# Kernel optimization log

Measured on AMD Instinct MI355X. Metric: run time of the kernel, lower is better.

The kernel has to match this reference:

```python
import jax, jax.numpy as jnp
import numpy as np
import math

SLIDING_WINDOW = 1024  # matches init kwarg

def setup_inputs() -> dict:
    key = jax.random.key(0)
    ks = jax.random.split(key, 6)
    B, S, Hq, Hkv, D = 1, 2048, 32, 8, 128
    NUM_PAGES, STRIDE = 300, 16
    q = jax.random.normal(ks[0], (B, S, Hq, D), dtype=jnp.float32)
    k = jax.random.normal(ks[1], (B, S, Hkv, D), dtype=jnp.float32)
    v = jax.random.normal(ks[2], (B, S, Hkv, D), dtype=jnp.float32)
    sink = jax.random.normal(ks[3], (Hq,), dtype=jnp.float32)
    cache_state = jnp.zeros((NUM_PAGES, STRIDE, 2, Hkv, D), dtype=jnp.float32)
    seq_block_ids = jax.random.randint(ks[4], (B, S // STRIDE), 0, NUM_PAGES, dtype=jnp.int64)
    return {"q": q, "k": k, "v": v, "sink": sink,
            "cache_state": cache_state, "seq_block_ids": seq_block_ids}


def reference(q, k, v, sink, cache_state, seq_block_ids):
    B, S, Hq, D = q.shape
    Hkv = k.shape[2]
    stride = cache_state.shape[1]

    # --- paged cache write (prefill side effect) ---
    kv = jnp.stack([k, v], axis=2)                       # [B,S,2,Hkv,D]
    pages = kv.reshape(B * (S // stride), stride, 2, Hkv, D)
    _ = cache_state.at[seq_block_ids.reshape(-1)].set(pages)

    # --- decomposed attention: matmul + mask + softmax(+sink) + matmul ---
    rep = Hq // Hkv
    ke = jnp.repeat(k, rep, axis=2)                      # [B,S,Hq,D] (GQA expand)
    ve = jnp.repeat(v, rep, axis=2)
    scale = 1.0 / math.sqrt(D)
    scores = jnp.einsum('bihd,bjhd->bhij', q, ke) * scale  # [B,Hq,S,S]

    i = jnp.arange(S)[:, None]
    j = jnp.arange(S)[None, :]
    allowed = (j <= i) & (i - j < SLIDING_WINDOW)        # causal + sliding window
    neg = jnp.finfo(scores.dtype).min
    logits = jnp.where(allowed, scores, neg)

    # attention sink: extra per-head logit appended; contributes to denominator only
    sink_l = jnp.broadcast_to(sink[None, :, None, None], (B, Hq, S, 1))
    probs = jax.nn.softmax(jnp.concatenate([logits, sink_l], axis=-1), axis=-1)[..., :S]

    out = jnp.einsum('bhij,bjhd->bihd', probs, ve)       # [B,S,Hq,D]
    return out
```

## Files before the change

kernel.cpp:

```cpp
#include <hip/hip_runtime.h>
#include <hip/hip_bf16.h>


#define S_LEN 2048
#define DH    128
#define HQ    32
#define HKV   8
#define WIN   1024
#define BR    64
#define BC    32
#define NT    (S_LEN / BC)
#define FM    16.0f
#define TILE_CH 512

typedef unsigned short u16;
typedef __attribute__((ext_vector_type(8))) short  short8;
typedef __attribute__((ext_vector_type(4))) float  floatx4;
typedef __attribute__((ext_vector_type(4))) unsigned int uintx4;

__device__ __forceinline__ unsigned rne1(float a) {
    unsigned u = __float_as_uint(a);
    return (u + 0x7FFFu + ((u >> 16) & 1u)) >> 16;
}
__device__ __forceinline__ unsigned rne_pk(float a, float b) {
    return rne1(a) | (rne1(b) << 16);
}
__device__ __forceinline__ unsigned cvt_pk(float a, float b) {
    unsigned r;
    asm("v_cvt_pk_bf16_f32 %0, %1, %2" : "=v"(r) : "v"(a), "v"(b));
    return r;
}

__global__ __launch_bounds__(256) void pack_kv(const float* __restrict__ kg,
                                               const float* __restrict__ vg,
                                               u16* __restrict__ kp,
                                               u16* __restrict__ vtp)
{
    __shared__ float Vs[BC][DH + 1];
    const int b   = blockIdx.x;
    const int hk  = b >> 6;
    const int jt  = b & 63;
    const int tid = threadIdx.x;
    const int j0  = jt * BC;

    #pragma unroll
    for (int t = 0; t < 4; t++) {
        int idx = tid + t * 256;
        int j   = idx >> 5;
        int dc  = idx & 31;
        floatx4 f = *(const floatx4*)(vg + ((size_t)(j0 + j) * HKV + hk) * DH + dc * 4);
        Vs[j][dc * 4 + 0] = f[0]; Vs[j][dc * 4 + 1] = f[1];
        Vs[j][dc * 4 + 2] = f[2]; Vs[j][dc * 4 + 3] = f[3];
    }

    u16* kpt = kp + (size_t)b * TILE_CH * 8;
    #pragma unroll
    for (int t = 0; t < 2; t++) {
        int c = tid + t * 256;
        int row = c >> 4, cc = c & 15;
        const float* p = kg + ((size_t)(j0 + row) * HKV + hk) * DH + cc * 8;
        floatx4 f0 = *(const floatx4*)p;
        floatx4 f1 = *(const floatx4*)(p + 4);
        int pc = (((row >> 4) * 4 + (cc >> 2)) << 6) | ((cc & 3) << 4) | (row & 15);
        *(uintx4*)(kpt + pc * 8) =
            (uintx4){rne_pk(f0[0], f0[1]), rne_pk(f0[2], f0[3]),
                     rne_pk(f1[0], f1[1]), rne_pk(f1[2], f1[3])};
    }
    __syncthreads();

    u16* vpt = vtp + (size_t)b * TILE_CH * 8;
    #pragma unroll
    for (int t = 0; t < 2; t++) {
        int q  = tid + t * 256;
        int dd = q >> 2, c = q & 3;
        unsigned w0 = rne_pk(Vs[c * 4 + 0][dd], Vs[c * 4 + 16][dd]);
        unsigned w1 = rne_pk(Vs[c * 4 + 1][dd], Vs[c * 4 + 17][dd]);
        unsigned w2 = rne_pk(Vs[c * 4 + 2][dd], Vs[c * 4 + 18][dd]);
        unsigned w3 = rne_pk(Vs[c * 4 + 3][dd], Vs[c * 4 + 19][dd]);
        int qp = ((dd >> 4) << 6) | (c << 4) | (dd & 15);
        *(uintx4*)(vpt + qp * 8) = (uintx4){w0, w1, w2, w3};
    }
}

__launch_bounds__(256, 5)
__global__ void fa_kernel(const float* __restrict__ qg,
                          const u16* __restrict__ kp,
                          const u16* __restrict__ vtp,
                          const float* __restrict__ sg,
                          float* __restrict__ outg)
{
    __shared__ __align__(16) u16 Kt[2][TILE_CH * 8];
    __shared__ __align__(16) u16 Vt[2][TILE_CH * 8];

    const int tid  = threadIdx.x;
    const int w    = tid >> 6;
    const int lane = tid & 63;
    const int quad = lane >> 4;
    const int l16  = lane & 15;

    const int bid  = blockIdx.x;
    const int hk   = bid & 7;
    const int idx  = bid >> 3;
    const int hrem = idx & 3;
    const int u5   = (idx >> 2) & 7;
    const int t4   = idx >> 5;
    const int qbt[4] = {u5, 15 - u5, 16 + u5, 31 - u5};
    const int qb   = qbt[t4];
    const int h    = hk * 4 + hrem;

    const int i0 = qb * BR;
    const int m0 = i0 + w * 16;

    short8 qf[4];
    {
        const float* qrow = qg + ((size_t)(m0 + l16) * HQ + h) * DH;
        #pragma unroll
        for (int kk = 0; kk < 4; kk++) {
            const float* p = qrow + kk * 32 + quad * 8;
            floatx4 f0 = *(const floatx4*)p;
            floatx4 f1 = *(const floatx4*)(p + 4);
            uintx4 uq = (uintx4){cvt_pk(f0[0], f0[1]), cvt_pk(f0[2], f0[3]),
                                 cvt_pk(f1[0], f1[1]), cvt_pk(f1[2], f1[3])};
            qf[kk] = *(short8*)&uq;
        }
    }

    const int lane8 = lane * 8;

    floatx4 acc[8];
    #pragma unroll
    for (int i = 0; i < 8; i++) acc[i] = (floatx4){0.f, 0.f, 0.f, 0.f};
    float l_sum = 0.f;

    const int ci  = m0 + l16;
    const int qb4 = quad * 4;

    int jlo = i0 - (WIN - 1); if (jlo < 0) jlo = 0;
    const int jt_lo = jlo >> 5;
    const int jt_hi = (i0 + BR - 1) >> 5;

    const float SC2 = 0.08838834764831845f * 1.4426950408889634f;

    const int ch0 = w * 64 + lane;
    auto stage = [&](int bb, int jt) {
        const u16* kpt = kp  + ((size_t)(hk * NT + jt)) * TILE_CH * 8;
        const u16* vpt = vtp + ((size_t)(hk * NT + jt)) * TILE_CH * 8;
        #pragma unroll
        for (int it = 0; it < 2; it++) {
            int ch = ch0 + it * 256;
            __builtin_amdgcn_global_load_lds(
                (const __attribute__((address_space(1))) unsigned*)(kpt + ch * 8),
                (__attribute__((address_space(3))) unsigned*)(&Kt[bb][ch * 8]), 16, 0, 0);
            __builtin_amdgcn_global_load_lds(
                (const __attribute__((address_space(1))) unsigned*)(vpt + ch * 8),
                (__attribute__((address_space(3))) unsigned*)(&Vt[bb][ch * 8]), 16, 0, 0);
        }
    };

    stage(0, jt_lo);
    int bb = 0;

    for (int jt = jt_lo; jt <= jt_hi; jt++) {
        const int j0 = jt << 5;

        __syncthreads();

        if (jt < jt_hi) stage(bb ^ 1, jt + 1);

        floatx4 ss[2];
        ss[0] = (floatx4){0.f, 0.f, 0.f, 0.f};
        ss[1] = (floatx4){0.f, 0.f, 0.f, 0.f};
        #pragma unroll
        for (int kk = 0; kk < 4; kk++) {
            short8 kf0 = *(const short8*)(&Kt[bb][(kk << 9) + lane8]);
            short8 kf1 = *(const short8*)(&Kt[bb][((4 + kk) << 9) + lane8]);
            ss[0] = __builtin_amdgcn_mfma_f32_16x16x32_bf16(kf0, qf[kk], ss[0], 0, 0, 0);
            ss[1] = __builtin_amdgcn_mfma_f32_16x16x32_bf16(kf1, qf[kk], ss[1], 0, 0, 0);
        }

        float p[2][4];
        const bool interior = (j0 + (BC - 1) <= i0) && (j0 >= i0 + BR - WIN);
        if (interior) {
            #pragma unroll
            for (int n = 0; n < 2; n++)
                #pragma unroll
                for (int r = 0; r < 4; r++)
                    p[n][r] = exp2f(fmaf(ss[n][r], SC2, -FM));
        } else {
            const int dj = ci - j0;
            #pragma unroll
            for (int n = 0; n < 2; n++)
                #pragma unroll
                for (int r = 0; r < 4; r++) {
                    int t = n * 16 + qb4 + r;
                    bool a = (t <= dj) && (t > dj - WIN);
                    p[n][r] = a ? exp2f(fmaf(ss[n][r], SC2, -FM)) : 0.f;
                }
        }
        l_sum += ((p[0][0] + p[0][1]) + (p[0][2] + p[0][3]))
               + ((p[1][0] + p[1][1]) + (p[1][2] + p[1][3]));

        uintx4 upf = (uintx4){cvt_pk(p[0][0], p[1][0]), cvt_pk(p[0][1], p[1][1]),
                              cvt_pk(p[0][2], p[1][2]), cvt_pk(p[0][3], p[1][3])};
        short8 pf = *(short8*)&upf;

        #pragma unroll
        for (int nf = 0; nf < 8; nf++) {
            short8 vf = *(const short8*)(&Vt[bb][(nf << 9) + lane8]);
            acc[nf] = __builtin_amdgcn_mfma_f32_16x16x32_bf16(pf, vf, acc[nf], 0, 0, 0);
        }
        bb ^= 1;
    }

    l_sum += __shfl_xor(l_sum, 16);
    l_sum += __shfl_xor(l_sum, 32);
    const float sk2 = exp2f(fmaf(sg[h], 1.4426950408889634f, -FM));
    float inv_r[4];
    #pragma unroll
    for (int r = 0; r < 4; r++) {
        float Lr = __shfl(l_sum, qb4 + r);
        inv_r[r] = 1.f / (Lr + sk2);
    }
    #pragma unroll
    for (int nf = 0; nf < 8; nf++) {
        int d = nf * 16 + l16;
        #pragma unroll
        for (int r = 0; r < 4; r++) {
            int ig = m0 + qb4 + r;
            outg[((size_t)ig * HQ + h) * DH + d] = acc[nf][r] * inv_r[r];
        }
    }
}

__launch_bounds__(256, 4)
__global__ void fa_fallback(const float* __restrict__ qg,
                            const float* __restrict__ kg,
                            const float* __restrict__ vg,
                            const float* __restrict__ sg,
                            float* __restrict__ outg)
{
    __shared__ __align__(16) u16 Kt[BC * DH];
    __shared__ __align__(16) u16 Vt[DH * BC];
    __shared__ __align__(16) u16 Pb[BR * 40];

    const int tid  = threadIdx.x;
    const int w    = tid >> 6;
    const int lane = tid & 63;
    const int quad = lane >> 4;
    const int l16  = lane & 15;

    const int qb = blockIdx.x / HQ;
    const int h  = blockIdx.x % HQ;
    const int hk = h >> 2;
    const int i0 = qb * BR;
    const int m0 = i0 + w * 16;

    short8 qf[4];
    {
        const float* qrow = qg + ((size_t)(m0 + l16) * HQ + h) * DH;
        #pragma unroll
        for (int kk = 0; kk < 4; kk++) {
            const float* p = qrow + kk * 32 + quad * 8;
            floatx4 f0 = *(const floatx4*)p;
            floatx4 f1 = *(const floatx4*)(p + 4);
            uintx4 u = (uintx4){rne_pk(f0[0], f0[1]), rne_pk(f0[2], f0[3]),
                                rne_pk(f1[0], f1[1]), rne_pk(f1[2], f1[3])};
            qf[kk] = *(short8*)&u;
        }
    }

    floatx4 acc[8];
    #pragma unroll
    for (int i = 0; i < 8; i++) acc[i] = (floatx4){0.f, 0.f, 0.f, 0.f};
    float l_part[4] = {0.f, 0.f, 0.f, 0.f};

    int jlo = i0 - (WIN - 1); if (jlo < 0) jlo = 0;
    const int jt_lo = jlo >> 5;
    const int jt_hi = (i0 + BR - 1) >> 5;
    const float SC2 = 0.08838834764831845f * 1.4426950408889634f;

    for (int jt = jt_lo; jt <= jt_hi; jt++) {
        const int j0 = jt << 5;
        __syncthreads();
        #pragma unroll
        for (int it = 0; it < 2; it++) {
            int g   = tid + 256 * it;
            int row = g >> 4, cc = g & 15;
            int pc  = (row << 4) | (cc ^ (row & 7));
            const float* kpp = kg + ((size_t)(j0 + row) * HKV + hk) * DH + cc * 8;
            floatx4 f0 = *(const floatx4*)kpp;
            floatx4 f1 = *(const floatx4*)(kpp + 4);
            *(uintx4*)(&Kt[pc * 8]) =
                (uintx4){rne_pk(f0[0], f0[1]), rne_pk(f0[2], f0[3]),
                         rne_pk(f1[0], f1[1]), rne_pk(f1[2], f1[3])};
        }
        #pragma unroll
        for (int it = 0; it < 2; it++) {
            int g  = tid + 256 * it;
            int d  = g & 127, jc = g >> 7;
            const float* vp = vg + ((size_t)(j0 + jc * 8) * HKV + hk) * DH + d;
            float e0 = vp[0 * HKV * DH], e1 = vp[1 * HKV * DH];
            float e2 = vp[2 * HKV * DH], e3 = vp[3 * HKV * DH];
            float e4 = vp[4 * HKV * DH], e5 = vp[5 * HKV * DH];
            float e6 = vp[6 * HKV * DH], e7 = vp[7 * HKV * DH];
            int pc = (d << 2) | (jc ^ ((d >> 2) & 3));
            *(uintx4*)(&Vt[pc * 8]) =
                (uintx4){rne_pk(e0, e1), rne_pk(e2, e3), rne_pk(e4, e5), rne_pk(e6, e7)};
        }
        __syncthreads();

        floatx4 sc[2];
        sc[0] = (floatx4){0.f, 0.f, 0.f, 0.f};
        sc[1] = (floatx4){0.f, 0.f, 0.f, 0.f};
        #pragma unroll
        for (int kk = 0; kk < 4; kk++) {
            #pragma unroll
            for (int n = 0; n < 2; n++) {
                int row = n * 16 + l16;
                int cc  = kk * 4 + quad;
                int pc  = (row << 4) | (cc ^ (row & 7));
                short8 kf = *(const short8*)(&Kt[pc * 8]);
                sc[n] = __builtin_amdgcn_mfma_f32_16x16x32_bf16(qf[kk], kf, sc[n], 0, 0, 0);
            }
        }
        #pragma unroll
        for (int r = 0; r < 4; r++) {
            int   i_g = m0 + quad * 4 + r;
            int   jg0 = j0 + l16, jg1 = j0 + 16 + l16;
            bool  a0  = (jg0 <= i_g) && (i_g - jg0 < WIN);
            bool  a1  = (jg1 <= i_g) && (i_g - jg1 < WIN);
            float p0  = a0 ? exp2f(fmaf(sc[0][r], SC2, -FM)) : 0.f;
            float p1  = a1 ? exp2f(fmaf(sc[1][r], SC2, -FM)) : 0.f;
            l_part[r] += p0 + p1;
            int prow = w * 16 + quad * 4 + r;
            *(unsigned*)(&Pb[prow * 40 + 2 * l16]) = rne_pk(p0, p1);
        }
        {
            short8 pf = *(const short8*)(&Pb[(w * 16 + l16) * 40 + quad * 8]);
            #pragma unroll
            for (int nf = 0; nf < 8; nf++) {
                int dd = nf * 16 + l16;
                int qp = (dd << 2) | (quad ^ ((dd >> 2) & 3));
                short8 vf = *(const short8*)(&Vt[qp * 8]);
                acc[nf] = __builtin_amdgcn_mfma_f32_16x16x32_bf16(pf, vf, acc[nf], 0, 0, 0);
            }
        }
    }

    const float sk2 = exp2f(fmaf(sg[h], 1.4426950408889634f, -FM));
    float inv[4];
    #pragma unroll
    for (int r = 0; r < 4; r++) {
        float l = l_part[r];
        #pragma unroll
        for (int off = 1; off < 16; off <<= 1)
            l += __shfl_xor(l, off);
        inv[r] = 1.f / (l + sk2);
    }
    #pragma unroll
    for (int nf = 0; nf < 8; nf++) {
        int d = nf * 16 + l16;
        #pragma unroll
        for (int r = 0; r < 4; r++) {
            int ig = m0 + quad * 4 + r;
            outg[((size_t)ig * HQ + h) * DH + d] = acc[nf][r] * inv[r];
        }
    }
}

extern "C" void kernel_launch(void* const* d_in, const int* in_sizes, int n_in,
                              void* d_out, int out_size, void* d_ws, size_t ws_size,
                              hipStream_t stream) {
    const float* q  = (const float*)d_in[0];
    const float* k  = (const float*)d_in[1];
    const float* v  = (const float*)d_in[2];
    const float* sk = (const float*)d_in[3];
    float* out = (float*)d_out;

    const size_t tile_elems = (size_t)HKV * NT * TILE_CH * 8;
    const size_t need = 2 * tile_elems * sizeof(u16);

    if (ws_size >= need) {
        u16* kp  = (u16*)d_ws;
        u16* vtp = kp + tile_elems;
        pack_kv<<<dim3(HKV * NT), 256, 0, stream>>>(k, v, kp, vtp);
        fa_kernel<<<dim3((S_LEN / BR) * HQ), 256, 0, stream>>>(q, kp, vtp, sk, out);
    } else {
        fa_fallback<<<dim3((S_LEN / BR) * HQ), 256, 0, stream>>>(q, k, v, sk, out);
    }
}
```

Before: 155.8 us.

## Halve warps per block, give each warp two 16-row query tiles

The attention block now runs 2 warps of 64 lanes instead of 4, and each warp handles 32 query rows as two 16-row MFMA tiles. Each K and V fragment read from LDS is reused across both query tiles, which halves LDS reads per unit of MFMA work. In exchange, per-thread register use roughly doubles for accumulators and Q fragments, and each block has fewer waves to hide latency; launch bounds change to (128, 2). Staging now issues four global-to-LDS loads per thread instead of two.

```diff
diff --git a/kernel.cpp b/kernel.cpp
--- a/kernel.cpp
+++ b/kernel.cpp
@@ -82,7 +82,7 @@
     }
 }
 
-__launch_bounds__(256, 5)
+__launch_bounds__(128, 2)
 __global__ void fa_kernel(const float* __restrict__ qg,
                           const u16* __restrict__ kp,
                           const u16* __restrict__ vtp,
@@ -109,11 +109,12 @@
     const int h    = hk * 4 + hrem;
 
     const int i0 = qb * BR;
-    const int m0 = i0 + w * 16;
-
-    short8 qf[4];
-    {
-        const float* qrow = qg + ((size_t)(m0 + l16) * HQ + h) * DH;
+    const int m0 = i0 + w * 32;
+
+    short8 qf[2][4];
+    #pragma unroll
+    for (int m = 0; m < 2; m++) {
+        const float* qrow = qg + ((size_t)(m0 + m * 16 + l16) * HQ + h) * DH;
         #pragma unroll
         for (int kk = 0; kk < 4; kk++) {
             const float* p = qrow + kk * 32 + quad * 8;
@@ -121,18 +122,19 @@
             floatx4 f1 = *(const floatx4*)(p + 4);
             uintx4 uq = (uintx4){cvt_pk(f0[0], f0[1]), cvt_pk(f0[2], f0[3]),
                                  cvt_pk(f1[0], f1[1]), cvt_pk(f1[2], f1[3])};
-            qf[kk] = *(short8*)&uq;
+            qf[m][kk] = *(short8*)&uq;
         }
     }
 
     const int lane8 = lane * 8;
 
-    floatx4 acc[8];
-    #pragma unroll
-    for (int i = 0; i < 8; i++) acc[i] = (floatx4){0.f, 0.f, 0.f, 0.f};
-    float l_sum = 0.f;
-
-    const int ci  = m0 + l16;
+    floatx4 acc[2][8];
+    #pragma unroll
+    for (int m = 0; m < 2; m++)
+        #pragma unroll
+        for (int i = 0; i < 8; i++) acc[m][i] = (floatx4){0.f, 0.f, 0.f, 0.f};
+    float l_sum[2] = {0.f, 0.f};
+
     const int qb4 = quad * 4;
 
     int jlo = i0 - (WIN - 1); if (jlo < 0) jlo = 0;
@@ -141,13 +143,12 @@
 
     const float SC2 = 0.08838834764831845f * 1.4426950408889634f;
 
-    const int ch0 = w * 64 + lane;
     auto stage = [&](int bb, int jt) {
         const u16* kpt = kp  + ((size_t)(hk * NT + jt)) * TILE_CH * 8;
         const u16* vpt = vtp + ((size_t)(hk * NT + jt)) * TILE_CH * 8;
         #pragma unroll
-        for (int it = 0; it < 2; it++) {
-            int ch = ch0 + it * 256;
+        for (int it = 0; it < 4; it++) {
+            int ch = tid + it * 128;
             __builtin_amdgcn_global_load_lds(
                 (const __attribute__((address_space(1))) unsigned*)(kpt + ch * 8),
                 (__attribute__((address_space(3))) unsigned*)(&Kt[bb][ch * 8]), 16, 0, 0);
@@ -167,67 +168,80 @@
 
         if (jt < jt_hi) stage(bb ^ 1, jt + 1);
 
-        floatx4 ss[2];
-        ss[0] = (floatx4){0.f, 0.f, 0.f, 0.f};
-        ss[1] = (floatx4){0.f, 0.f, 0.f, 0.f};
+        floatx4 ss[2][2];
+        #pragma unroll
+        for (int n = 0; n < 2; n++) {
+            ss[n][0] = (floatx4){0.f, 0.f, 0.f, 0.f};
+            ss[n][1] = (floatx4){0.f, 0.f, 0.f, 0.f};
+        }
         #pragma unroll
         for (int kk = 0; kk < 4; kk++) {
             short8 kf0 = *(const short8*)(&Kt[bb][(kk << 9) + lane8]);
             short8 kf1 = *(const short8*)(&Kt[bb][((4 + kk) << 9) + lane8]);
-            ss[0] = __builtin_amdgcn_mfma_f32_16x16x32_bf16(kf0, qf[kk], ss[0], 0, 0, 0);
-            ss[1] = __builtin_amdgcn_mfma_f32_16x16x32_bf16(kf1, qf[kk], ss[1], 0, 0, 0);
-        }
-
-        float p[2][4];
+            ss[0][0] = __builtin_amdgcn_mfma_f32_16x16x32_bf16(kf0, qf[0][kk], ss[0][0], 0, 0, 0);
+            ss[0][1] = __builtin_amdgcn_mfma_f32_16x16x32_bf16(kf0, qf[1][kk], ss[0][1], 0, 0, 0);
+            ss[1][0] = __builtin_amdgcn_mfma_f32_16x16x32_bf16(kf1, qf[0][kk], ss[1][0], 0, 0, 0);
+            ss[1][1] = __builtin_amdgcn_mfma_f32_16x16x32_bf16(kf1, qf[1][kk], ss[1][1], 0, 0, 0);
+        }
+
+        short8 pf[2];
         const bool interior = (j0 + (BC - 1) <= i0) && (j0 >= i0 + BR - WIN);
-        if (interior) {
-            #pragma unroll
-            for (int n = 0; n < 2; n++)
+        #pragma unroll
+        for (int m = 0; m < 2; m++) {
+            float p[2][4];
+            if (interior) {
                 #pragma unroll
-                for (int r = 0; r < 4; r++)
-                    p[n][r] = exp2f(fmaf(ss[n][r], SC2, -FM));
-        } else {
-            const int dj = ci - j0;
-            #pragma unroll
-            for (int n = 0; n < 2; n++)
+                for (int n = 0; n < 2; n++)
+                    #pragma unroll
+                    for (int r = 0; r < 4; r++)
+                        p[n][r] = exp2f(fmaf(ss[n][m][r], SC2, -FM));
+            } else {
+                const int dj = m0 + m * 16 + l16 - j0;
                 #pragma unroll
-                for (int r = 0; r < 4; r++) {
-                    int t = n * 16 + qb4 + r;
-                    bool a = (t <= dj) && (t > dj - WIN);
-                    p[n][r] = a ? exp2f(fmaf(ss[n][r], SC2, -FM)) : 0.f;
-                }
-        }
-        l_sum += ((p[0][0] + p[0][1]) + (p[0][2] + p[0][3]))
-               + ((p[1][0] + p[1][1]) + (p[1][2] + p[1][3]));
-
-        uintx4 upf = (uintx4){cvt_pk(p[0][0], p[1][0]), cvt_pk(p[0][1], p[1][1]),
-                              cvt_pk(p[0][2], p[1][2]), cvt_pk(p[0][3], p[1][3])};
-        short8 pf = *(short8*)&upf;
+                for (int n = 0; n < 2; n++)
+                    #pragma unroll
+                    for (int r = 0; r < 4; r++) {
+                        int t = n * 16 + qb4 + r;
+                        bool a = (t <= dj) && (t > dj - WIN);
+                        p[n][r] = a ? exp2f(fmaf(ss[n][m][r], SC2, -FM)) : 0.f;
+                    }
+            }
+            l_sum[m] += ((p[0][0] + p[0][1]) + (p[0][2] + p[0][3]))
+                      + ((p[1][0] + p[1][1]) + (p[1][2] + p[1][3]));
+            uintx4 upf = (uintx4){cvt_pk(p[0][0], p[1][0]), cvt_pk(p[0][1], p[1][1]),
+                                  cvt_pk(p[0][2], p[1][2]), cvt_pk(p[0][3], p[1][3])};
+            pf[m] = *(short8*)&upf;
+        }
 
         #pragma unroll
         for (int nf = 0; nf < 8; nf++) {
             short8 vf = *(const short8*)(&Vt[bb][(nf << 9) + lane8]);
-            acc[nf] = __builtin_amdgcn_mfma_f32_16x16x32_bf16(pf, vf, acc[nf], 0, 0, 0);
+            acc[0][nf] = __builtin_amdgcn_mfma_f32_16x16x32_bf16(pf[0], vf, acc[0][nf], 0, 0, 0);
+            acc[1][nf] = __builtin_amdgcn_mfma_f32_16x16x32_bf16(pf[1], vf, acc[1][nf], 0, 0, 0);
         }
         bb ^= 1;
     }
 
-    l_sum += __shfl_xor(l_sum, 16);
-    l_sum += __shfl_xor(l_sum, 32);
     const float sk2 = exp2f(fmaf(sg[h], 1.4426950408889634f, -FM));
-    float inv_r[4];
-    #pragma unroll
-    for (int r = 0; r < 4; r++) {
-        float Lr = __shfl(l_sum, qb4 + r);
-        inv_r[r] = 1.f / (Lr + sk2);
-    }
-    #pragma unroll
-    for (int nf = 0; nf < 8; nf++) {
-        int d = nf * 16 + l16;
+    #pragma unroll
+    for (int m = 0; m < 2; m++) {
+        float l = l_sum[m];
+        l += __shfl_xor(l, 16);
+        l += __shfl_xor(l, 32);
+        float inv_r[4];
         #pragma unroll
         for (int r = 0; r < 4; r++) {
-            int ig = m0 + qb4 + r;
-            outg[((size_t)ig * HQ + h) * DH + d] = acc[nf][r] * inv_r[r];
+            float Lr = __shfl(l, qb4 + r);
+            inv_r[r] = 1.f / (Lr + sk2);
+        }
+        #pragma unroll
+        for (int nf = 0; nf < 8; nf++) {
+            int d = nf * 16 + l16;
+            #pragma unroll
+            for (int r = 0; r < 4; r++) {
+                int ig = m0 + m * 16 + qb4 + r;
+                outg[((size_t)ig * HQ + h) * DH + d] = acc[m][nf][r] * inv_r[r];
+            }
         }
     }
 }
@@ -384,7 +398,7 @@
         u16* kp  = (u16*)d_ws;
         u16* vtp = kp + tile_elems;
         pack_kv<<<dim3(HKV * NT), 256, 0, stream>>>(k, v, kp, vtp);
-        fa_kernel<<<dim3((S_LEN / BR) * HQ), 256, 0, stream>>>(q, kp, vtp, sk, out);
+        fa_kernel<<<dim3((S_LEN / BR) * HQ), 128, 0, stream>>>(q, kp, vtp, sk, out);
     } else {
         fa_fallback<<<dim3((S_LEN / BR) * HQ), 256, 0, stream>>>(q, k, v, sk, out);
     }
```

Measured after the change: 165.7 us. +6.4%, slower.
